# Kernel optimization log

Hardware: AMD Instinct MI355X
Metric: run time of the kernel (lower is better)

The kernel has to match this reference:

```python
import jax, jax.numpy as jnp
import numpy as np

N, CIN, COUT, T, V, K = 32, 64, 64, 6, 512, 8
NEG_FILL = -1000.0  # value the torch code writes into masked scores
LEAKY_SLOPE = 0.2


def setup_inputs() -> dict:
    key = jax.random.key(0)
    ks = jax.random.split(key, 9)
    x = jax.random.normal(ks[0], (N, CIN, T, V), jnp.float32)
    # A: 7 'feature' channels (sliced off and unused in forward) + 1 binary mask channel
    A_feat = jax.random.normal(ks[1], (N, 7, V, V), jnp.float32)
    mask = (jax.random.uniform(ks[2], (N, 1, V, V)) < 0.7).astype(jnp.float32)
    A = jnp.concatenate([A_feat, mask], axis=1)  # [N, 8, V, V]
    # conv is a pointwise (1x1-in-time) Conv2d: weight [COUT, CIN]
    conv_w = jax.random.normal(ks[3], (COUT, CIN), jnp.float32) / np.float32(np.sqrt(CIN))
    conv_b = jax.random.normal(ks[4], (COUT,), jnp.float32) * 0.01
    # l2: Linear(6 -> 1) applied along time
    l2_w = jax.random.normal(ks[5], (T,), jnp.float32) / np.float32(np.sqrt(T))
    l2_b = jax.random.normal(ks[6], (1,), jnp.float32) * 0.01
    # l1: Linear(128 -> 1) applied to concat([x10_i, x10_j])
    l1_w = jax.random.normal(ks[7], (2 * COUT,), jnp.float32) / np.float32(np.sqrt(2 * COUT))
    l1_b = jax.random.normal(ks[8], (1,), jnp.float32) * 0.01
    return {"x": x, "A": A, "conv_w": conv_w, "conv_b": conv_b,
            "l1_w": l1_w, "l1_b": l1_b, "l2_w": l2_w, "l2_b": l2_b}


def reference(x, A, conv_w, conv_b, l1_w, l1_b, l2_w, l2_b):
    # pointwise conv over channels: [N,CIN,T,V] -> [N,COUT,T,V]
    xc = jnp.einsum('nitv,oi->notv', x, conv_w) + conv_b[None, :, None, None]
    mask = A[:, 7]  # [N,V,V]; channels 0..6 are sliced off and unused downstream
    # l2 collapses time: x10[n,v,c] = sum_t xc[n,c,t,v] * l2_w[t] + l2_b
    x10 = jnp.einsum('nctv,t->nvc', xc, l2_w) + l2_b
    # GAT-style pairwise score: l1(cat(x10[i], x10[j])) == s_i + s_j + b
    w_src, w_dst = l1_w[:COUT], l1_w[COUT:]
    s_i = x10 @ w_src  # [N,V]
    s_j = x10 @ w_dst  # [N,V]
    scores = s_i[:, :, None] + s_j[:, None, :] + l1_b  # [N,V,V]
    a1 = jax.nn.leaky_relu(scores, LEAKY_SLOPE)
    a2 = jnp.where(mask.astype(jnp.int32) == 0, jnp.float32(NEG_FILL), a1)
    a4 = jax.nn.softmax(a2, axis=2)  # softmax over second node index (torch dim=2)
    # einsum('nctv,ndvw->ncdtw') with d=1, then reshape -> [N,C,T,V]
    out = jnp.einsum('nctv,nvw->nctw', xc, a4)
    return out, a4[:, None]  # A6: [N,1,V,V]
```

## Files before the change

### kernel.cpp

```cpp
#include <hip/hip_runtime.h>
#include <hip/hip_bf16.h>
#include <stdint.h>

#define BN 32
#define CIN 64
#define COUTC 64
#define TT 6
#define VV 512
#define NEG_FILL -1000.0f
#define SLOPE 0.2f

using bf16x8 = __attribute__((ext_vector_type(8))) short;
using bf16x4 = __attribute__((ext_vector_type(4))) short;
using f32x4  = __attribute__((ext_vector_type(4))) float;

static __device__ __forceinline__ unsigned short f2bf(float f) {
    union { float f; unsigned int i; } x; x.f = f;
    unsigned int r = x.i + 0x7FFFu + ((x.i >> 16) & 1u);
    return (unsigned short)(r >> 16);
}

#define GLD16(gp, lp) __builtin_amdgcn_global_load_lds( \
    (const __attribute__((address_space(1))) void*)(gp), \
    (__attribute__((address_space(3))) void*)(lp), 16, 0, 0)

__global__ __launch_bounds__(256) void k1_conv(const float* __restrict__ x,
                                               const float* __restrict__ W,
                                               const float* __restrict__ bias,
                                               const float* __restrict__ l1w,
                                               const float* __restrict__ l2w,
                                               unsigned short* __restrict__ xcb,
                                               float* __restrict__ spartS,
                                               float* __restrict__ spartD) {
    __shared__ __align__(16) unsigned short Ws[64 * 64];
    __shared__ __align__(16) unsigned short Bs[128 * 64];
    int bid = blockIdx.x;
    int vq = bid & 3; int nt = bid >> 2; int t = nt % TT; int n = nt / TT;
    int tid = threadIdx.x; int wv = tid >> 6, ln = tid & 63;
    int v0 = vq * 128;

    {
        int o = tid >> 2, i16 = (tid & 3) * 16;
        const float* wr_ = W + o * CIN + i16;
        f32x4 a = *(const f32x4*)&wr_[0], b = *(const f32x4*)&wr_[4];
        f32x4 c = *(const f32x4*)&wr_[8], d = *(const f32x4*)&wr_[12];
        bf16x8 p0, p1;
        #pragma unroll
        for (int e = 0; e < 4; ++e) {
            p0[e] = (short)f2bf(a[e]); p0[e + 4] = (short)f2bf(b[e]);
            p1[e] = (short)f2bf(c[e]); p1[e + 4] = (short)f2bf(d[e]);
        }
        int j0 = i16 >> 3;
        *(bf16x8*)&Ws[o * 64 + ((j0 ^ (o & 7)) << 3)]       = p0;
        *(bf16x8*)&Ws[o * 64 + (((j0 + 1) ^ (o & 7)) << 3)] = p1;
    }
    const float* xg = x + ((size_t)(n * CIN) * TT + t) * VV + v0;
    {
        int v4 = (tid & 31) * 4;
        int ig0 = tid >> 5;
        #pragma unroll
        for (int g = 0; g < 2; ++g) {
            int i4 = (ig0 + g * 8) * 4;
            f32x4 r0 = *(const f32x4*)&xg[(size_t)(i4 + 0) * TT * VV + v4];
            f32x4 r1 = *(const f32x4*)&xg[(size_t)(i4 + 1) * TT * VV + v4];
            f32x4 r2 = *(const f32x4*)&xg[(size_t)(i4 + 2) * TT * VV + v4];
            f32x4 r3 = *(const f32x4*)&xg[(size_t)(i4 + 3) * TT * VV + v4];
            int j = i4 >> 3, h = (i4 >> 2) & 1;
            #pragma unroll
            for (int c = 0; c < 4; ++c) {
                int v = v4 + c;
                bf16x4 col;
                col[0] = (short)f2bf(r0[c]); col[1] = (short)f2bf(r1[c]);
                col[2] = (short)f2bf(r2[c]); col[3] = (short)f2bf(r3[c]);
                *(bf16x4*)&Bs[v * 64 + ((j ^ (v & 7)) << 3) + h * 4] = col;
            }
        }
    }
    __syncthreads();

    int fr = ln & 15, fkq = ln >> 4;
    f32x4 acc[4][2] = {};
    #pragma unroll
    for (int ks = 0; ks < 2; ++ks) {
        bf16x8 af[4], bfv[2];
        int oct = fkq + ks * 4;
        #pragma unroll
        for (int mi = 0; mi < 4; ++mi) {
            int o = mi * 16 + fr;
            af[mi] = *(const bf16x8*)&Ws[o * 64 + ((oct ^ (o & 7)) << 3)];
        }
        #pragma unroll
        for (int ni = 0; ni < 2; ++ni) {
            int v = wv * 32 + ni * 16 + fr;
            bfv[ni] = *(const bf16x8*)&Bs[v * 64 + ((oct ^ (v & 7)) << 3)];
        }
        #pragma unroll
        for (int mi = 0; mi < 4; ++mi)
            #pragma unroll
            for (int ni = 0; ni < 2; ++ni)
                acc[mi][ni] = __builtin_amdgcn_mfma_f32_16x16x32_bf16(af[mi], bfv[ni], acc[mi][ni], 0, 0, 0);
    }
    __syncthreads();

    float l2wt = l2w[t];
    float partS[2] = {0.f, 0.f}, partD[2] = {0.f, 0.f};
    #pragma unroll
    for (int mi = 0; mi < 4; ++mi)
        #pragma unroll
        for (int q = 0; q < 4; ++q) {
            int o = mi * 16 + (ln >> 4) * 4 + q;
            float bv = bias[o];
            float wS = l1w[o], wD = l1w[COUTC + o];
            #pragma unroll
            for (int ni = 0; ni < 2; ++ni) {
                float z = acc[mi][ni][q] + bv;
                partS[ni] += wS * z;
                partD[ni] += wD * z;
                int vloc = wv * 32 + ni * 16 + fr;
                int vsw = (((vloc >> 3) ^ (o & 15)) << 3) | (vloc & 7);
                Bs[o * 128 + vsw] = f2bf(z);
            }
        }
    #pragma unroll
    for (int ni = 0; ni < 2; ++ni) {
        float sS = partS[ni], sD = partD[ni];
        sS += __shfl_xor(sS, 16); sS += __shfl_xor(sS, 32);
        sD += __shfl_xor(sD, 16); sD += __shfl_xor(sD, 32);
        if (ln < 16) {
            int v = v0 + wv * 32 + ni * 16 + ln;
            size_t si_ = ((size_t)n * TT + t) * VV + v;
            spartS[si_] = l2wt * sS;
            spartD[si_] = l2wt * sD;
        }
    }
    __syncthreads();

    {
        int o = tid >> 2, c32 = (tid & 3) * 32;
        size_t base = ((size_t)(n * COUTC + o) * TT + t) * VV + v0 + c32;
        #pragma unroll
        for (int q = 0; q < 4; ++q) {
            int oct = (tid & 3) * 4 + q;
            bf16x8 val = *(const bf16x8*)&Bs[o * 128 + ((oct ^ (o & 15)) << 3)];
            *(bf16x8*)&xcb[base + q * 8] = val;
        }
    }
}

__global__ __launch_bounds__(256) void k2_softmax(const float* __restrict__ A,
                                                  const float* __restrict__ spartS,
                                                  const float* __restrict__ spartD,
                                                  const float* __restrict__ l1w,
                                                  const float* __restrict__ l1b_,
                                                  const float* __restrict__ l2b_,
                                                  float* __restrict__ a4out,
                                                  unsigned short* __restrict__ a4t) {
    __shared__ unsigned short tile[32][520];
    __shared__ float si_loc[32];
    int blk = blockIdx.x;
    int n = blk >> 4; int i0 = (blk & 15) * 32;
    int wv = threadIdx.x >> 6, lane = threadIdx.x & 63;

    float sws = 0.f, swd = 0.f;
    for (int c = 0; c < COUTC; ++c) { sws += l1w[c]; swd += l1w[COUTC + c]; }
    float l2b = l2b_[0], l1b = l1b_[0];

    if (threadIdx.x < 32) {
        float s = 0.f;
        #pragma unroll
        for (int t = 0; t < TT; ++t)
            s += spartS[((size_t)n * TT + t) * VV + i0 + threadIdx.x];
        si_loc[threadIdx.x] = s + l2b * sws;
    }
    f32x4 sj0 = {0.f, 0.f, 0.f, 0.f}, sj1 = {0.f, 0.f, 0.f, 0.f};
    #pragma unroll
    for (int t = 0; t < TT; ++t) {
        const float* p = &spartD[((size_t)n * TT + t) * VV + lane * 8];
        f32x4 d0 = *(const f32x4*)&p[0];
        f32x4 d1 = *(const f32x4*)&p[4];
        #pragma unroll
        for (int e = 0; e < 4; ++e) { sj0[e] += d0[e]; sj1[e] += d1[e]; }
    }
    float cst = l2b * swd + l1b;
    #pragma unroll
    for (int e = 0; e < 4; ++e) { sj0[e] += cst; sj1[e] += cst; }
    __syncthreads();

    for (int it = 0; it < 8; ++it) {
        int il = it * 4 + wv;
        int i  = i0 + il;
        int row = n * VV + i;
        float s_i = si_loc[il];
        const float* mrow = A + ((size_t)n * 8 + 7) * VV * VV + (size_t)i * VV;
        f32x4 m0 = *(const f32x4*)&mrow[lane * 8];
        f32x4 m1 = *(const f32x4*)&mrow[lane * 8 + 4];

        float sc[8];
        float mx = -1e30f;
        #pragma unroll
        for (int e = 0; e < 8; ++e) {
            float mk = (e < 4) ? m0[e] : m1[e - 4];
            float s  = s_i + ((e < 4) ? sj0[e] : sj1[e - 4]);
            s = (s >= 0.f) ? s : SLOPE * s;
            s = (mk == 0.f) ? NEG_FILL : s;
            sc[e] = s;
            mx = fmaxf(mx, s);
        }
        #pragma unroll
        for (int off = 32; off; off >>= 1) mx = fmaxf(mx, __shfl_xor(mx, off));
        float sum = 0.f;
        #pragma unroll
        for (int e = 0; e < 8; ++e) { sc[e] = __expf(sc[e] - mx); sum += sc[e]; }
        #pragma unroll
        for (int off = 32; off; off >>= 1) sum += __shfl_xor(sum, off);
        float inv = 1.f / sum;
        f32x4 o0, o1;
        bf16x8 pk;
        #pragma unroll
        for (int e = 0; e < 4; ++e) {
            o0[e] = sc[e] * inv; o1[e] = sc[e + 4] * inv;
            pk[e]     = (short)f2bf(o0[e]);
            pk[e + 4] = (short)f2bf(o1[e]);
        }
        *(f32x4*)&a4out[(size_t)row * VV + lane * 8]     = o0;
        *(f32x4*)&a4out[(size_t)row * VV + lane * 8 + 4] = o1;
        *(bf16x8*)&tile[il][lane * 8] = pk;
    }
    __syncthreads();

    int i4    = (threadIdx.x & 7) * 4;
    int wbase = threadIdx.x >> 3;
    unsigned short* dst = a4t + (size_t)n * VV * VV + i0;
    #pragma unroll
    for (int ws = 0; ws < 16; ++ws) {
        int w = ws * 32 + wbase;
        ushort4 val;
        val.x = tile[i4 + 0][w];
        val.y = tile[i4 + 1][w];
        val.z = tile[i4 + 2][w];
        val.w = tile[i4 + 3][w];
        *(ushort4*)&dst[(size_t)w * VV + i4] = val;
    }
}

__global__ __launch_bounds__(512) void k3_gemm(const unsigned short* __restrict__ xcb,
                                               const unsigned short* __restrict__ a4t,
                                               float* __restrict__ outp) {
    __shared__ __align__(16) unsigned short As[2][128 * 32];
    __shared__ __align__(16) unsigned short Bs[2][128 * 32];

    int bid = blockIdx.x;
    int n = bid / 12; int s = bid % 12; int rt = s >> 2, wt_ = s & 3;
    int r0 = rt * 128, w0 = wt_ * 128;
    int tid = threadIdx.x; int wv = tid >> 6, ln = tid & 63;
    int wr = wv >> 2, wc = wv & 3;
    const unsigned short* Ag = xcb + (size_t)n * (COUTC * TT) * VV;
    const unsigned short* Bg = a4t + (size_t)n * VV * VV;

    int fr  = ln & 15;
    int fkq = ln >> 4;
    int row_l = tid >> 2;
    int sw_st = (((tid & 3) ^ ((row_l >> 1) & 3)) << 3);

    f32x4 acc[4][2] = {};

#define STAGE(bsel, kt) do {                                                        \
        int k0_ = (kt) * 32;                                                        \
        GLD16(Ag + (size_t)(r0 + row_l) * VV + k0_ + sw_st,                         \
              &As[bsel][(wv * 16) * 32]);                                           \
        GLD16(Bg + (size_t)(w0 + row_l) * VV + k0_ + sw_st,                         \
              &Bs[bsel][(wv * 16) * 32]);                                           \
    } while (0)

    STAGE(0, 0);
    __syncthreads();

    for (int kt = 0; kt < 16; ++kt) {
        int cur = kt & 1;
        if (kt < 15) STAGE(cur ^ 1, kt + 1);

        bf16x8 af[4], bfv[2];
        #pragma unroll
        for (int mi = 0; mi < 4; ++mi) {
            int r = wr * 64 + mi * 16 + fr;
            af[mi] = *(const bf16x8*)&As[cur][r * 32 + ((fkq ^ ((r >> 1) & 3)) << 3)];
        }
        #pragma unroll
        for (int ni = 0; ni < 2; ++ni) {
            int w = wc * 32 + ni * 16 + fr;
            bfv[ni] = *(const bf16x8*)&Bs[cur][w * 32 + ((fkq ^ ((w >> 1) & 3)) << 3)];
        }
        #pragma unroll
        for (int ni = 0; ni < 2; ++ni)
            #pragma unroll
            for (int mi = 0; mi < 4; ++mi)
                acc[mi][ni] = __builtin_amdgcn_mfma_f32_16x16x32_bf16(af[mi], bfv[ni], acc[mi][ni], 0, 0, 0);

        __syncthreads();
    }
#undef STAGE

    float* og = outp + (size_t)n * (COUTC * TT) * VV;
    #pragma unroll
    for (int mi = 0; mi < 4; ++mi) {
        int rbase = r0 + wr * 64 + mi * 16 + (ln >> 4) * 4;
        #pragma unroll
        for (int ni = 0; ni < 2; ++ni) {
            int col = w0 + wc * 32 + ni * 16 + (ln & 15);
            #pragma unroll
            for (int q = 0; q < 4; ++q)
                og[(size_t)(rbase + q) * VV + col] = acc[mi][ni][q];
        }
    }
}

extern "C" void kernel_launch(void* const* d_in, const int* in_sizes, int n_in,
                              void* d_out, int out_size, void* d_ws, size_t ws_size,
                              hipStream_t stream) {
    const float* x      = (const float*)d_in[0];
    const float* A      = (const float*)d_in[1];
    const float* conv_w = (const float*)d_in[2];
    const float* conv_b = (const float*)d_in[3];
    const float* l1w    = (const float*)d_in[4];
    const float* l1b    = (const float*)d_in[5];
    const float* l2w    = (const float*)d_in[6];
    const float* l2b    = (const float*)d_in[7];

    float* outp  = (float*)d_out;
    float* a4out = outp + (size_t)BN * COUTC * TT * VV;

    unsigned short* xcb = (unsigned short*)d_ws;
    unsigned short* a4t = xcb + (size_t)BN * COUTC * TT * VV;
    float* spartS = (float*)(a4t + (size_t)BN * VV * VV);
    float* spartD = spartS + (size_t)BN * TT * VV;

    k1_conv    <<<BN * TT * 4, 256, 0, stream>>>(x, conv_w, conv_b, l1w, l2w, xcb, spartS, spartD);
    k2_softmax <<<BN * 16, 256, 0, stream>>>(A, spartS, spartD, l1w, l1b, l2b, a4out, a4t);
    k3_gemm    <<<BN * 12, 512, 0, stream>>>(xcb, a4t, outp);
}
```

Baseline: 53.72 us.

## Retile batched GEMM to 64x128 with K=64 stages and remap block order

The output GEMM now uses 256-thread blocks, each computing a 64x128 tile with 64-wide K steps and an XOR swizzle over 8 groups. The grid doubles to 768 blocks, and the block index is permuted so that consecutive blocks are spread across batches, which may help L2 or XCD locality. The softmax kernel moves to 512 threads so that each wave handles fewer rows. The aim is better occupancy and load balance across CUs, at the cost of more redundant loads of the B operand per batch.

```diff
diff --git a/kernel.cpp b/kernel.cpp
--- a/kernel.cpp
+++ b/kernel.cpp
@@ -147,7 +147,7 @@
     }
 }
 
-__global__ __launch_bounds__(256) void k2_softmax(const float* __restrict__ A,
+__global__ __launch_bounds__(512) void k2_softmax(const float* __restrict__ A,
                                                   const float* __restrict__ spartS,
                                                   const float* __restrict__ spartD,
                                                   const float* __restrict__ l1w,
@@ -186,8 +186,8 @@
     for (int e = 0; e < 4; ++e) { sj0[e] += cst; sj1[e] += cst; }
     __syncthreads();
 
-    for (int it = 0; it < 8; ++it) {
-        int il = it * 4 + wv;
+    for (int it = 0; it < 4; ++it) {
+        int il = it * 8 + wv;
         int i  = i0 + il;
         int row = n * VV + i;
         float s_i = si_loc[il];
@@ -232,8 +232,8 @@
     int wbase = threadIdx.x >> 3;
     unsigned short* dst = a4t + (size_t)n * VV * VV + i0;
     #pragma unroll
-    for (int ws = 0; ws < 16; ++ws) {
-        int w = ws * 32 + wbase;
+    for (int ws = 0; ws < 8; ++ws) {
+        int w = ws * 64 + wbase;
         ushort4 val;
         val.x = tile[i4 + 0][w];
         val.y = tile[i4 + 1][w];
@@ -243,70 +243,81 @@
     }
 }
 
-__global__ __launch_bounds__(512) void k3_gemm(const unsigned short* __restrict__ xcb,
+__global__ __launch_bounds__(256) void k3_gemm(const unsigned short* __restrict__ xcb,
                                                const unsigned short* __restrict__ a4t,
                                                float* __restrict__ outp) {
-    __shared__ __align__(16) unsigned short As[2][128 * 32];
-    __shared__ __align__(16) unsigned short Bs[2][128 * 32];
-
-    int bid = blockIdx.x;
-    int n = bid / 12; int s = bid % 12; int rt = s >> 2, wt_ = s & 3;
-    int r0 = rt * 128, w0 = wt_ * 128;
+    __shared__ __align__(16) unsigned short As[2][64 * 64];
+    __shared__ __align__(16) unsigned short Bs[2][128 * 64];
+
+    int bid = (blockIdx.x & 7) * 96 + (blockIdx.x >> 3);
+    int n = bid / 24; int s = bid % 24; int rt = s >> 2, wt_ = s & 3;
+    int r0 = rt * 64, w0 = wt_ * 128;
     int tid = threadIdx.x; int wv = tid >> 6, ln = tid & 63;
-    int wr = wv >> 2, wc = wv & 3;
+    int wr = wv >> 1, wc = wv & 1;
     const unsigned short* Ag = xcb + (size_t)n * (COUTC * TT) * VV;
     const unsigned short* Bg = a4t + (size_t)n * VV * VV;
 
     int fr  = ln & 15;
     int fkq = ln >> 4;
-    int row_l = tid >> 2;
-    int sw_st = (((tid & 3) ^ ((row_l >> 1) & 3)) << 3);
-
-    f32x4 acc[4][2] = {};
-
-#define STAGE(bsel, kt) do {                                                        \
-        int k0_ = (kt) * 32;                                                        \
-        GLD16(Ag + (size_t)(r0 + row_l) * VV + k0_ + sw_st,                         \
-              &As[bsel][(wv * 16) * 32]);                                           \
-        GLD16(Bg + (size_t)(w0 + row_l) * VV + k0_ + sw_st,                         \
-              &Bs[bsel][(wv * 16) * 32]);                                           \
+    int st_row = tid >> 3;
+    int st_g   = tid & 7;
+
+    f32x4 acc[2][4] = {};
+
+#define STAGE(bsel, kt) do {                                                          \
+        int k0_ = (kt) * 64;                                                          \
+        _Pragma("unroll")                                                             \
+        for (int c2 = 0; c2 < 2; ++c2) {                                              \
+            int row = c2 * 32 + st_row;                                               \
+            GLD16(Ag + (size_t)(r0 + row) * VV + k0_ + ((st_g ^ (row & 7)) << 3),     \
+                  &As[bsel][c2 * 2048 + wv * 512]);                                   \
+        }                                                                             \
+        _Pragma("unroll")                                                             \
+        for (int c4 = 0; c4 < 4; ++c4) {                                              \
+            int row = c4 * 32 + st_row;                                               \
+            GLD16(Bg + (size_t)(w0 + row) * VV + k0_ + ((st_g ^ (row & 7)) << 3),     \
+                  &Bs[bsel][c4 * 2048 + wv * 512]);                                   \
+        }                                                                             \
     } while (0)
 
     STAGE(0, 0);
     __syncthreads();
 
-    for (int kt = 0; kt < 16; ++kt) {
+    for (int kt = 0; kt < 8; ++kt) {
         int cur = kt & 1;
-        if (kt < 15) STAGE(cur ^ 1, kt + 1);
-
-        bf16x8 af[4], bfv[2];
-        #pragma unroll
-        for (int mi = 0; mi < 4; ++mi) {
-            int r = wr * 64 + mi * 16 + fr;
-            af[mi] = *(const bf16x8*)&As[cur][r * 32 + ((fkq ^ ((r >> 1) & 3)) << 3)];
-        }
-        #pragma unroll
-        for (int ni = 0; ni < 2; ++ni) {
-            int w = wc * 32 + ni * 16 + fr;
-            bfv[ni] = *(const bf16x8*)&Bs[cur][w * 32 + ((fkq ^ ((w >> 1) & 3)) << 3)];
-        }
-        #pragma unroll
-        for (int ni = 0; ni < 2; ++ni)
-            #pragma unroll
-            for (int mi = 0; mi < 4; ++mi)
-                acc[mi][ni] = __builtin_amdgcn_mfma_f32_16x16x32_bf16(af[mi], bfv[ni], acc[mi][ni], 0, 0, 0);
-
+        if (kt < 7) STAGE(cur ^ 1, kt + 1);
+
+        #pragma unroll
+        for (int ks = 0; ks < 2; ++ks) {
+            int g = ks * 4 + fkq;
+            bf16x8 af[2], bfv[4];
+            #pragma unroll
+            for (int mi = 0; mi < 2; ++mi) {
+                int r = wr * 32 + mi * 16 + fr;
+                af[mi] = *(const bf16x8*)&As[cur][r * 64 + ((g ^ (r & 7)) << 3)];
+            }
+            #pragma unroll
+            for (int ni = 0; ni < 4; ++ni) {
+                int w = wc * 64 + ni * 16 + fr;
+                bfv[ni] = *(const bf16x8*)&Bs[cur][w * 64 + ((g ^ (w & 7)) << 3)];
+            }
+            #pragma unroll
+            for (int ni = 0; ni < 4; ++ni)
+                #pragma unroll
+                for (int mi = 0; mi < 2; ++mi)
+                    acc[mi][ni] = __builtin_amdgcn_mfma_f32_16x16x32_bf16(af[mi], bfv[ni], acc[mi][ni], 0, 0, 0);
+        }
         __syncthreads();
     }
 #undef STAGE
 
     float* og = outp + (size_t)n * (COUTC * TT) * VV;
     #pragma unroll
-    for (int mi = 0; mi < 4; ++mi) {
-        int rbase = r0 + wr * 64 + mi * 16 + (ln >> 4) * 4;
-        #pragma unroll
-        for (int ni = 0; ni < 2; ++ni) {
-            int col = w0 + wc * 32 + ni * 16 + (ln & 15);
+    for (int mi = 0; mi < 2; ++mi) {
+        int rbase = r0 + wr * 32 + mi * 16 + (ln >> 4) * 4;
+        #pragma unroll
+        for (int ni = 0; ni < 4; ++ni) {
+            int col = w0 + wc * 64 + ni * 16 + (ln & 15);
             #pragma unroll
             for (int q = 0; q < 4; ++q)
                 og[(size_t)(rbase + q) * VV + col] = acc[mi][ni][q];
@@ -335,6 +346,6 @@
     float* spartD = spartS + (size_t)BN * TT * VV;
 
     k1_conv    <<<BN * TT * 4, 256, 0, stream>>>(x, conv_w, conv_b, l1w, l2w, xcb, spartS, spartD);
-    k2_softmax <<<BN * 16, 256, 0, stream>>>(A, spartS, spartD, l1w, l1b, l2b, a4out, a4t);
-    k3_gemm    <<<BN * 12, 512, 0, stream>>>(xcb, a4t, outp);
-}
+    k2_softmax <<<BN * 16, 512, 0, stream>>>(A, spartS, spartD, l1w, l1b, l2b, a4out, a4t);
+    k3_gemm    <<<BN * 24, 256, 0, stream>>>(xcb, a4t, outp);
+}
```

Result: faster. 47.57 us (-11.4%).
